# Optimization experiments

Measured on AMD Instinct MI355X. Metric: run time of the kernel, lower is better.

## Reference

```python
import jax, jax.numpy as jnp
import numpy as np

B, G, T, N = 4, 8, 30, 60
CT, CN = 1, 60
FD, IDD = 256, 256
E = FD + IDD          # 512
H = 8                 # (FD+IDD)//head_dim
L = 6                 # num_layers
VP1 = 51              # num_id_vocabulary + 1
PE = 32               # rel_pe_length
DFF = 4 * E


def _ln(x, g, b, eps=1e-5):
    m = x.mean(-1, keepdims=True)
    v = ((x - m) ** 2).mean(-1, keepdims=True)
    return (x - m) / jnp.sqrt(v + eps) * g + b


def _mha(qx, kx, vx, Wqkv, bqkv, Wo, bo, bias, h):
    # torch nn.MultiheadAttention with add_zero_attn=True; bias is additive
    # attn bias of shape [B, h, Lq, Lk+1] (already padded for the zero-attn col).
    e = qx.shape[-1]
    d = e // h
    Wq, Wk, Wv = jnp.split(Wqkv, 3, axis=0)
    bq, bk, bv = jnp.split(bqkv, 3)
    q = qx @ Wq.T + bq
    k = kx @ Wk.T + bk
    v = vx @ Wv.T + bv
    b_, lq, _ = q.shape
    lk = k.shape[1]
    z = jnp.zeros((b_, 1, e), q.dtype)
    k = jnp.concatenate([k, z], axis=1)   # add_zero_attn appends zero key
    v = jnp.concatenate([v, z], axis=1)
    qh = q.reshape(b_, lq, h, d).transpose(0, 2, 1, 3)
    kh = k.reshape(b_, lk + 1, h, d).transpose(0, 2, 1, 3)
    vh = v.reshape(b_, lk + 1, h, d).transpose(0, 2, 1, 3)
    s = jnp.einsum('bhqd,bhkd->bhqk', qh, kh) / jnp.sqrt(jnp.float32(d)) + bias
    p = jax.nn.softmax(s, axis=-1)
    o = jnp.einsum('bhqk,bhkd->bhqd', p, vh).transpose(0, 2, 1, 3).reshape(b_, lq, e)
    return o @ Wo.T + bo


def _forward(tf, uf, ids, tt_, ut_, tm, um, Ww, Wout, rpe,
             saW, sab, saO, saob, sag, sabn,
             caW, cab, caO, caob, cag, cabn,
             f1, fb1, f2, fb2, fg, fbn):
    b, g, t, n, fd = tf.shape
    _, _, ct, cn, _ = uf.shape
    id_dim = Ww.shape[0]
    e = fd + id_dim
    nl = caW.shape[0]
    h = rpe.shape[-1]
    pe = rpe.shape[1]
    # one_hot(label) @ W_word.T == W_word[:, label]
    traj_id = Ww.T[ids]                                        # b g t n id
    unk_id = jnp.broadcast_to(Ww[:, VP1 - 1], (b, g, ct, cn, id_dim))
    traj = jnp.concatenate([tf, traj_id], -1).reshape(b * g, t * n, e)
    unk = jnp.concatenate([uf, unk_id], -1)                    # b g ct cn e

    tt = tt_.reshape(b * g, t * n)
    ut = ut_.reshape(b * g, ct * cn)
    neg = jnp.float32(-jnp.inf)
    zero = jnp.float32(0)
    causal = jnp.where(tt[:, None, :] >= ut[:, :, None], neg, zero)  # bg q k
    kpm = jnp.where(tm.reshape(b * g, t * n), neg, zero)             # bg k
    # torch rel_pos_map[u, t] = u - t; negative torch indices wrap -> mod pe
    rel_idx = (ut[:, :, None] - tt[:, None, :]) % pe                 # bg q k
    sa_bias = jnp.pad(
        jnp.where(um.reshape(b * g * ct, cn), neg, zero)[:, None, None, :],
        ((0, 0), (0, 0), (0, 0), (0, 1)))

    for l in range(nl):
        if l > 0:
            x = unk.reshape(b * g * ct, cn, e)
            y = _mha(x, x, x, saW[l - 1], sab[l - 1], saO[l - 1], saob[l - 1], sa_bias, h)
            unk = _ln(x + y, sag[l - 1], sabn[l - 1]).reshape(b, g, ct, cn, e)
        q = unk.reshape(b * g, ct * cn, e)
        rel = rpe[l][rel_idx]                                  # bg q k h  (gathered rel-PE)
        bias = causal[:, None] + jnp.transpose(rel, (0, 3, 1, 2)) + kpm[:, None, None, :]
        bias = jnp.pad(bias, ((0, 0), (0, 0), (0, 0), (0, 1)))
        y = _mha(q, traj, traj, caW[l], cab[l], caO[l], caob[l], bias, h)
        x = _ln(q + y, cag[l], cabn[l])
        hh = jax.nn.gelu(x @ f1[l].T + fb1[l], approximate=False) @ f2[l].T + fb2[l]
        x = _ln(x + hh, fg[l], fbn[l])
        unk = x.reshape(b, g, ct, cn, e)
    # final layer logits (eval mode): shared embed_to_word head, no bias
    return unk[..., fd:] @ Wout.T


def setup_inputs():
    key = jax.random.key(0)
    ks = iter(jax.random.split(key, 48))
    nrm = lambda shape, s=0.02: jax.random.normal(next(ks), shape, jnp.float32) * s
    return {
        'trajectory_features': jax.random.normal(next(ks), (B, G, T, N, FD), jnp.float32),
        'unknown_features': jax.random.normal(next(ks), (B, G, CT, CN, FD), jnp.float32),
        'trajectory_id_labels': jax.random.randint(next(ks), (B, G, T, N), 0, VP1),
        'trajectory_times': jax.random.randint(next(ks), (B, G, T, N), 0, PE),
        'unknown_times': jax.random.randint(next(ks), (B, G, CT, CN), 0, PE),
        'trajectory_masks': jnp.zeros((B, G, T, N), bool),
        'unknown_masks': jnp.zeros((B, G, CT, CN), bool),
        'use_decoder_checkpoint': 0,
        'W_word': nrm((IDD, VP1), 0.05),
        'W_out': nrm((VP1, IDD), 0.05),
        'rel_pos_embeds': nrm((L, PE, H), 0.1),
        'sa_Wqkv': nrm((L - 1, 3 * E, E)), 'sa_bqkv': jnp.zeros((L - 1, 3 * E)),
        'sa_Wo': nrm((L - 1, E, E)), 'sa_bo': jnp.zeros((L - 1, E)),
        'sa_ln_g': jnp.ones((L - 1, E)), 'sa_ln_b': jnp.zeros((L - 1, E)),
        'ca_Wqkv': nrm((L, 3 * E, E)), 'ca_bqkv': jnp.zeros((L, 3 * E)),
        'ca_Wo': nrm((L, E, E)), 'ca_bo': jnp.zeros((L, E)),
        'ca_ln_g': jnp.ones((L, E)), 'ca_ln_b': jnp.zeros((L, E)),
        'ffn_W1': nrm((L, DFF, E)), 'ffn_b1': jnp.zeros((L, DFF)),
        'ffn_W2': nrm((L, E, DFF)), 'ffn_b2': jnp.zeros((L, E)),
        'ffn_ln_g': jnp.ones((L, E)), 'ffn_ln_b': jnp.zeros((L, E)),
    }


def reference(trajectory_features, unknown_features, trajectory_id_labels,
              trajectory_times, unknown_times, trajectory_masks, unknown_masks,
              use_decoder_checkpoint, W_word, W_out, rel_pos_embeds,
              sa_Wqkv, sa_bqkv, sa_Wo, sa_bo, sa_ln_g, sa_ln_b,
              ca_Wqkv, ca_bqkv, ca_Wo, ca_bo, ca_ln_g, ca_ln_b,
              ffn_W1, ffn_b1, ffn_W2, ffn_b2, ffn_ln_g, ffn_ln_b):
    return _forward(trajectory_features, unknown_features, trajectory_id_labels,
                    trajectory_times, unknown_times, trajectory_masks, unknown_masks,
                    W_word, W_out, rel_pos_embeds,
                    sa_Wqkv, sa_bqkv, sa_Wo, sa_bo, sa_ln_g, sa_ln_b,
                    ca_Wqkv, ca_bqkv, ca_Wo, ca_bo, ca_ln_g, ca_ln_b,
                    ffn_W1, ffn_b1, ffn_W2, ffn_b2, ffn_ln_g, ffn_ln_b)
```

## Files before the change

### kernel.cpp

```cpp
#include <hip/hip_runtime.h>
#include <cmath>

__device__ __forceinline__ float bflo(unsigned int u) {
  union { unsigned int i; float f; } v; v.i = u << 16; return v.f;
}
__device__ __forceinline__ float bfhi(unsigned int u) {
  union { unsigned int i; float f; } v; v.i = u & 0xffff0000u; return v.f;
}
__device__ __forceinline__ float bf2f(unsigned short u) {
  union { unsigned int i; float f; } v; v.i = ((unsigned int)u) << 16; return v.f;
}
__device__ __forceinline__ unsigned short f2bf(float f) {
  union { float f; unsigned int i; } v; v.f = f;
  unsigned int i = v.i;
  return (unsigned short)((i + 0x7fffu + ((i >> 16) & 1u)) >> 16);
}
__device__ __forceinline__ unsigned int pack2bf(float a, float b) {
  return (unsigned int)f2bf(a) | ((unsigned int)f2bf(b) << 16);
}

typedef __attribute__((ext_vector_type(8))) short short8;
typedef __attribute__((ext_vector_type(4))) float floatx4;

__global__ __launch_bounds__(256) void conv_kernel(
    const float* __restrict__ in, unsigned short* __restrict__ out, int n)
{
  int i = (blockIdx.x * 256 + threadIdx.x) << 2;
  if (i >= n) return;
  float4 v = *reinterpret_cast<const float4*>(in + i);
  ushort4 o;
  o.x = f2bf(v.x); o.y = f2bf(v.y); o.z = f2bf(v.z); o.w = f2bf(v.w);
  *reinterpret_cast<ushort4*>(out + i) = o;
}

__global__ __launch_bounds__(256) void build_wwt_kernel(
    const float* __restrict__ Ww, unsigned short* __restrict__ Wwt)
{
  int c = blockIdx.x;
  int r = threadIdx.x;
  Wwt[c * 256 + r] = f2bf(Ww[r * 51 + c]);
}

__global__ __launch_bounds__(512, 4) void gemm256(
    const unsigned short* __restrict__ A,
    const unsigned short* __restrict__ W,
    const float* __restrict__ bias,
    unsigned short* __restrict__ C)
{
  __shared__ __align__(16) unsigned short LA[2][4096];
  __shared__ __align__(16) unsigned short LB[2][8192];
  const int tid = threadIdx.x;
  const int wave = tid >> 6, lane = tid & 63;
  const int quad = lane >> 4, mrow = lane & 15;
  const int wm = wave >> 2, wn = wave & 3;
  const size_t ldK = 512;
  const int nt = 16;

  int f = blockIdx.x;
  {
    const int q = gridDim.x >> 3;
    f = (f & 7) * q + (f >> 3);
  }
  const int bn = (f & 3) << 8;
  const int bm = (f >> 2) << 7;

  floatx4 acc[4][4];
#pragma unroll
  for (int i = 0; i < 4; ++i)
#pragma unroll
    for (int j = 0; j < 4; ++j) acc[i][j] = (floatx4){0.f, 0.f, 0.f, 0.f};

  const int srow = tid >> 2;
  const int sslot = (tid & 3) ^ ((srow >> 1) & 3);

#define STAGE32(p, kelem)                                                            \
  do {                                                                               \
    __builtin_amdgcn_global_load_lds(                                                \
        (const __attribute__((address_space(1))) unsigned int*)(                     \
            A + (size_t)(bm + srow) * ldK + (kelem) + sslot * 8),                    \
        (__attribute__((address_space(3))) unsigned int*)(&LA[(p)][0] + wave * 512), \
        16, 0, 0);                                                                   \
    __builtin_amdgcn_global_load_lds(                                                \
        (const __attribute__((address_space(1))) unsigned int*)(                     \
            W + (size_t)(bn + srow) * ldK + (kelem) + sslot * 8),                    \
        (__attribute__((address_space(3))) unsigned int*)(&LB[(p)][0] + wave * 512), \
        16, 0, 0);                                                                   \
    __builtin_amdgcn_global_load_lds(                                                \
        (const __attribute__((address_space(1))) unsigned int*)(                     \
            W + (size_t)(bn + 128 + srow) * ldK + (kelem) + sslot * 8),              \
        (__attribute__((address_space(3))) unsigned int*)(&LB[(p)][4096] + wave * 512), \
        16, 0, 0);                                                                   \
  } while (0)

  STAGE32(0, 0);
  STAGE32(1, 32);
  asm volatile("s_waitcnt vmcnt(3)" ::: "memory");
  __builtin_amdgcn_s_barrier();

  const int rsw = ((quad ^ ((mrow >> 1) & 3)) << 3);
  const int arowb = wm * 64 + mrow;
  const int brows = wn * 64 + mrow;

  for (int T = 0; T < nt; ++T) {
    const int p = T & 1;
    short8 afr[4], bfr[4];
#pragma unroll
    for (int i = 0; i < 4; ++i)
      afr[i] = *reinterpret_cast<const short8*>(&LA[p][(arowb + i * 16) * 32 + rsw]);
#pragma unroll
    for (int j = 0; j < 4; ++j)
      bfr[j] = *reinterpret_cast<const short8*>(&LB[p][(brows + j * 16) * 32 + rsw]);
    asm volatile("s_waitcnt lgkmcnt(0)" ::: "memory");
    __builtin_amdgcn_s_barrier();
    if (T + 2 < nt) STAGE32(p, (T + 2) * 32);
    __builtin_amdgcn_s_setprio(1);
#pragma unroll
    for (int i = 0; i < 4; ++i)
#pragma unroll
      for (int j = 0; j < 4; ++j)
        acc[i][j] = __builtin_amdgcn_mfma_f32_16x16x32_bf16(afr[i], bfr[j], acc[i][j], 0, 0, 0);
    __builtin_amdgcn_s_setprio(0);
    if (T + 2 < nt) asm volatile("s_waitcnt vmcnt(3)" ::: "memory");
    else            asm volatile("s_waitcnt vmcnt(0)" ::: "memory");
    __builtin_amdgcn_s_barrier();
  }
#undef STAGE32

  const int col0 = lane & 15;
  const int row0 = (lane >> 4) << 2;
#pragma unroll
  for (int i = 0; i < 4; ++i)
#pragma unroll
    for (int j = 0; j < 4; ++j) {
      int col = bn + wn * 64 + j * 16 + col0;
      float bv = bias[col];
#pragma unroll
      for (int r = 0; r < 4; ++r) {
        int row = bm + wm * 64 + i * 16 + row0 + r;
        C[(size_t)row * 1024 + col] = f2bf(acc[i][j][r] + bv);
      }
    }
}

__global__ __launch_bounds__(256) void gemm_mfma(
    const unsigned short* __restrict__ A, int lda,
    const unsigned short* __restrict__ W, int ldw,
    const float* __restrict__ bias,
    void* __restrict__ Cv, int ldc,
    int K, int act, int cbf16, int swz)
{
  __shared__ __align__(16) unsigned short As[2][128 * 32];
  __shared__ __align__(16) unsigned short Bs[2][128 * 32];
  const int tid = threadIdx.x;
  const int wave = tid >> 6, lane = tid & 63;

  int bxi = blockIdx.x, byi = blockIdx.y;
  if (swz) {
    int f = byi * gridDim.x + bxi;
    int q = (gridDim.x * gridDim.y) >> 3;
    f = (f & 7) * q + (f >> 3);
    bxi = f % gridDim.x;
    byi = f / gridDim.x;
  }
  const int bm = byi * 128, bn = bxi * 128;
  const int wm = (wave >> 1) << 6, wn = (wave & 1) << 6;

  floatx4 acc[4][4];
#pragma unroll
  for (int i = 0; i < 4; ++i)
#pragma unroll
    for (int j = 0; j < 4; ++j) acc[i][j] = (floatx4){0.f, 0.f, 0.f, 0.f};

  const int srow = (wave << 5) + (lane >> 2);
  const int chsw = (lane & 3) ^ ((srow >> 1) & 3);
  const int scol = chsw << 3;
  const unsigned short* Ag  = A + (size_t)(bm + srow) * lda + scol;
  const unsigned short* Wg  = W + (size_t)(bn + srow) * ldw + scol;
  const unsigned short* Ag2 = Ag + (size_t)16 * lda;
  const unsigned short* Wg2 = Wg + (size_t)16 * ldw;
  const int ldsw = (wave << 5) * 32;

  const int arow = lane & 15;
  const int rsw  = (arow >> 1) & 3;
  const int chrd = (lane >> 4) ^ rsw;
  const int aoff = (wm + arow) * 32 + (chrd << 3);
  const int boff = (wn + arow) * 32 + (chrd << 3);

  const int nt = K >> 5;

#define STAGE(b, t)                                                                 \
  do {                                                                              \
    const int k0_ = (t) << 5;                                                       \
    __builtin_amdgcn_global_load_lds(                                               \
        (const __attribute__((address_space(1))) unsigned int*)(Ag + k0_),          \
        (__attribute__((address_space(3))) unsigned int*)(As[(b)] + ldsw), 16, 0, 0); \
    __builtin_amdgcn_global_load_lds(                                               \
        (const __attribute__((address_space(1))) unsigned int*)(Ag2 + k0_),         \
        (__attribute__((address_space(3))) unsigned int*)(As[(b)] + ldsw + 16 * 32), 16, 0, 0); \
    __builtin_amdgcn_global_load_lds(                                               \
        (const __attribute__((address_space(1))) unsigned int*)(Wg + k0_),          \
        (__attribute__((address_space(3))) unsigned int*)(Bs[(b)] + ldsw), 16, 0, 0); \
    __builtin_amdgcn_global_load_lds(                                               \
        (const __attribute__((address_space(1))) unsigned int*)(Wg2 + k0_),         \
        (__attribute__((address_space(3))) unsigned int*)(Bs[(b)] + ldsw + 16 * 32), 16, 0, 0); \
  } while (0)

  STAGE(0, 0);
  if (nt > 1) STAGE(1, 1);

  int cur = 0;
  for (int t = 0; t < nt; ++t) {
    if (t + 1 < nt) asm volatile("s_waitcnt vmcnt(4)\n\ts_barrier" ::: "memory");
    else            asm volatile("s_waitcnt vmcnt(0)\n\ts_barrier" ::: "memory");

    short8 af[4], bf[4];
#pragma unroll
    for (int i = 0; i < 4; ++i) {
      af[i] = *reinterpret_cast<const short8*>(&As[cur][aoff + (i << 4) * 32]);
      bf[i] = *reinterpret_cast<const short8*>(&Bs[cur][boff + (i << 4) * 32]);
    }
    asm volatile("s_waitcnt lgkmcnt(0)\n\ts_barrier" ::: "memory");
    if (t + 2 < nt) STAGE(cur, t + 2);

#pragma unroll
    for (int i = 0; i < 4; ++i)
#pragma unroll
      for (int j = 0; j < 4; ++j)
        acc[i][j] = __builtin_amdgcn_mfma_f32_16x16x32_bf16(af[i], bf[j], acc[i][j], 0, 0, 0);
    cur ^= 1;
  }
#undef STAGE

  const int col0 = lane & 15;
  const int row0 = (lane >> 4) << 2;
#pragma unroll
  for (int i = 0; i < 4; ++i) {
#pragma unroll
    for (int j = 0; j < 4; ++j) {
      int col = bn + wn + (j << 4) + col0;
      float bv = bias ? bias[col] : 0.f;
#pragma unroll
      for (int r = 0; r < 4; ++r) {
        int row = bm + wm + (i << 4) + row0 + r;
        float v = acc[i][j][r] + bv;
        if (act) v = 0.5f * v * (1.f + erff(v * 0.70710678f));
        if (cbf16) ((unsigned short*)Cv)[(size_t)row * ldc + col] = f2bf(v);
        else       ((float*)Cv)[(size_t)row * ldc + col] = v;
      }
    }
  }
}

__device__ __forceinline__ float wred_max(float v) {
#pragma unroll
  for (int off = 32; off > 0; off >>= 1) v = fmaxf(v, __shfl_xor(v, off, 64));
  return v;
}
__device__ __forceinline__ float wred_sum(float v) {
#pragma unroll
  for (int off = 32; off > 0; off >>= 1) v += __shfl_xor(v, off, 64);
  return v;
}

#define LDK 72
__global__ __launch_bounds__(512) void attn_mfma_kernel(
    const unsigned short* __restrict__ Qp,
    const unsigned short* __restrict__ KVb,
    unsigned short* __restrict__ O,
    const int* __restrict__ tt, const int* __restrict__ ut,
    const unsigned char* __restrict__ km,
    const float* __restrict__ rel)
{
  const int bg = blockIdx.x >> 3, h = blockIdx.x & 7;
  const int tid = threadIdx.x;
  const int grp = tid >> 8;
  const int wave = (tid >> 6) & 3;
  const int lane = tid & 63;
  const int quad = lane >> 4, mrow = lane & 15;

  __shared__ __align__(16) unsigned short SMEM[6 * 64 * LDK];
  unsigned short* Ks = SMEM + grp * (3 * 64 * LDK);
  unsigned short* Vt = Ks + 64 * LDK;
  unsigned short* Ps = Vt + 64 * LDK;

  const int qa = wave * 16 + mrow;
  const int qc = qa < 60 ? qa : 59;
  const unsigned short* qptr = Qp + (size_t)(bg * 60 + qc) * 512 + h * 64 + quad * 8;
  const short8 af0 = *reinterpret_cast<const short8*>(qptr);
  const short8 af1 = *reinterpret_cast<const short8*>(qptr + 32);

  const float relreg = rel[(lane & 31) * 8 + h];

  int tq[4];
  float m[4], l[4];
  floatx4 acc[4];
#pragma unroll
  for (int r = 0; r < 4; ++r) {
    int qo = wave * 16 + quad * 4 + r;
    tq[r] = ut[bg * 60 + (qo < 60 ? qo : 59)];
    m[r] = grp ? -1e30f : 0.f;
    l[r] = grp ? 0.f : 1.f;
  }
#pragma unroll
  for (int nt = 0; nt < 4; ++nt) acc[nt] = (floatx4){0.f, 0.f, 0.f, 0.f};

  const int sk = tid & 255;
  const int stok = sk >> 2, schk = sk & 3;

  for (int it = 0; it < 15; ++it) {
    const int k0 = (grp + 2 * it) << 6;
    __syncthreads();
    {
      const int key = k0 + stok;
      uint4 kr0 = {0,0,0,0}, kr1 = {0,0,0,0}, vr0 = {0,0,0,0}, vr1 = {0,0,0,0};
      if (key < 1800) {
        const unsigned short* kb = KVb + ((size_t)bg * 1800 + key) * 1024 + h * 64 + schk * 16;
        kr0 = *reinterpret_cast<const uint4*>(kb);
        kr1 = *reinterpret_cast<const uint4*>(kb + 8);
        vr0 = *reinterpret_cast<const uint4*>(kb + 512);
        vr1 = *reinterpret_cast<const uint4*>(kb + 520);
      }
      *reinterpret_cast<uint4*>(&Ks[stok * LDK + schk * 16]) = kr0;
      *reinterpret_cast<uint4*>(&Ks[stok * LDK + schk * 16 + 8]) = kr1;
      unsigned int wv[8] = {vr0.x, vr0.y, vr0.z, vr0.w, vr1.x, vr1.y, vr1.z, vr1.w};
#pragma unroll
      for (int e = 0; e < 16; ++e)
        Vt[(schk * 16 + e) * LDK + stok] = (unsigned short)(wv[e >> 1] >> ((e & 1) * 16));
    }
    int meta = 0x10000;
    {
      int kk = k0 + lane;
      if (kk < 1800) {
        int base = bg * 1800 + kk;
        meta = tt[base] | (km[base] ? 0x10000 : 0);
      }
    }
    __syncthreads();

    floatx4 S[4];
#pragma unroll
    for (int nt = 0; nt < 4; ++nt) {
      const unsigned short* kb = Ks + (nt * 16 + mrow) * LDK + quad * 8;
      short8 b0 = *reinterpret_cast<const short8*>(kb);
      short8 b1 = *reinterpret_cast<const short8*>(kb + 32);
      floatx4 s = (floatx4){0.f, 0.f, 0.f, 0.f};
      s = __builtin_amdgcn_mfma_f32_16x16x32_bf16(af0, b0, s, 0, 0, 0);
      s = __builtin_amdgcn_mfma_f32_16x16x32_bf16(af1, b1, s, 0, 0, 0);
      S[nt] = s;
    }
    int mcol[4];
#pragma unroll
    for (int nt = 0; nt < 4; ++nt)
      mcol[nt] = __builtin_amdgcn_ds_bpermute((nt * 16 + mrow) << 2, meta);
    float sv[4][4];
#pragma unroll
    for (int nt = 0; nt < 4; ++nt) {
      int tk = mcol[nt] & 0xffff;
      int bad0 = mcol[nt] >> 16;
#pragma unroll
      for (int r = 0; r < 4; ++r) {
        float v = S[nt][r] * 0.125f;
        int ridx = (tq[r] - tk) & 31;
        v += __int_as_float(__builtin_amdgcn_ds_bpermute(ridx << 2, __float_as_int(relreg)));
        sv[nt][r] = (bad0 | (tk >= tq[r])) ? -1e30f : v;
      }
    }
#pragma unroll
    for (int r = 0; r < 4; ++r) {
      float rm = fmaxf(fmaxf(sv[0][r], sv[1][r]), fmaxf(sv[2][r], sv[3][r]));
#pragma unroll
      for (int d = 1; d < 16; d <<= 1) rm = fmaxf(rm, __shfl_xor(rm, d, 64));
      float nm = fmaxf(m[r], rm);
      float corr = __expf(m[r] - nm);
      float ps = 0.f;
      const int prow = (wave * 16 + quad * 4 + r) * LDK + mrow;
#pragma unroll
      for (int nt = 0; nt < 4; ++nt) {
        float p = __expf(sv[nt][r] - nm);
        ps += p;
        Ps[prow + nt * 16] = f2bf(p);
      }
#pragma unroll
      for (int d = 1; d < 16; d <<= 1) ps += __shfl_xor(ps, d, 64);
      l[r] = l[r] * corr + ps;
      m[r] = nm;
#pragma unroll
      for (int nt = 0; nt < 4; ++nt) acc[nt][r] *= corr;
    }
    const unsigned short* pp = Ps + (wave * 16 + mrow) * LDK + quad * 8;
    short8 a0 = *reinterpret_cast<const short8*>(pp);
    short8 a1 = *reinterpret_cast<const short8*>(pp + 32);
#pragma unroll
    for (int nt = 0; nt < 4; ++nt) {
      const unsigned short* vb = Vt + (nt * 16 + mrow) * LDK + quad * 8;
      short8 b0 = *reinterpret_cast<const short8*>(vb);
      short8 b1 = *reinterpret_cast<const short8*>(vb + 32);
      acc[nt] = __builtin_amdgcn_mfma_f32_16x16x32_bf16(a0, b0, acc[nt], 0, 0, 0);
      acc[nt] = __builtin_amdgcn_mfma_f32_16x16x32_bf16(a1, b1, acc[nt], 0, 0, 0);
    }
  }

  __syncthreads();
  float* MA = (float*)SMEM;
  float* Ml = (float*)(SMEM + 64 * 68 * 2);
  float* Ll = Ml + 64;
  if (grp == 1) {
#pragma unroll
    for (int r = 0; r < 4; ++r) {
      int row = wave * 16 + quad * 4 + r;
#pragma unroll
      for (int nt = 0; nt < 4; ++nt)
        MA[row * 68 + nt * 16 + mrow] = acc[nt][r];
      if (mrow == 0) { Ml[row] = m[r]; Ll[row] = l[r]; }
    }
  }
  __syncthreads();
  if (grp == 0) {
#pragma unroll
    for (int r = 0; r < 4; ++r) {
      int row = wave * 16 + quad * 4 + r;
      float m1 = Ml[row], l1 = Ll[row];
      float M = fmaxf(m[r], m1);
      float c0 = __expf(m[r] - M), c1 = __expf(m1 - M);
      float invL = 1.f / (l[r] * c0 + l1 * c1);
      if (row < 60) {
        unsigned short* op = O + (size_t)(bg * 60 + row) * 512 + h * 64;
#pragma unroll
        for (int nt = 0; nt < 4; ++nt) {
          float o = (acc[nt][r] * c0 + MA[row * 68 + nt * 16 + mrow] * c1) * invL;
          op[nt * 16 + mrow] = f2bf(o);
        }
      }
    }
  }
}

#define QPB 32
#define QPW 8
__global__ __launch_bounds__(256) void attn2_kernel(
    const unsigned short* __restrict__ Qp, int qs,
    const unsigned short* __restrict__ Kp, int ks,
    const unsigned short* __restrict__ Vp, int vs,
    unsigned short* __restrict__ O, int os, int kLen,
    const unsigned char* __restrict__ kmask)
{
  const int bg = blockIdx.x >> 3;
  const int h  = blockIdx.x & 7;
  const int q0 = blockIdx.y * QPB;
  const int tid = threadIdx.x;
  const int wave = tid >> 6, lane = tid & 63;

  __shared__ float Qs[QPB][68];
  __shared__ float Ks[64][68];
  __shared__ float Vs[64][68];
  __shared__ float Ps[QPB][68];

  {
    int qr = tid >> 3, j = tid & 7;
    int q = q0 + qr;
    float f[8] = {0, 0, 0, 0, 0, 0, 0, 0};
    if (q < 60) {
      uint4 v = *reinterpret_cast<const uint4*>(Qp + (size_t)(bg * 60 + q) * qs + h * 64 + j * 8);
      f[0] = bflo(v.x); f[1] = bfhi(v.x); f[2] = bflo(v.y); f[3] = bfhi(v.y);
      f[4] = bflo(v.z); f[5] = bfhi(v.z); f[6] = bflo(v.w); f[7] = bfhi(v.w);
    }
#pragma unroll
    for (int e = 0; e < 8; ++e) Qs[qr][j * 8 + e] = f[e];
  }

  float m[QPW], l[QPW], acc[QPW];
#pragma unroll
  for (int i = 0; i < QPW; ++i) { m[i] = 0.f; l[i] = 1.f; acc[i] = 0.f; }

  const int std = tid >> 2;
  const int stj = tid & 3;

  for (int k0 = 0; k0 < kLen; k0 += 64) {
    __syncthreads();
    const bool sok = (k0 + std) < kLen;
    {
      const unsigned short* kb = Kp + ((size_t)bg * kLen + k0 + std) * ks + h * 64 + stj * 16;
      float f[16];
#pragma unroll
      for (int e = 0; e < 16; ++e) f[e] = 0.f;
      if (sok) {
        uint4 v0 = *reinterpret_cast<const uint4*>(kb);
        uint4 v1 = *reinterpret_cast<const uint4*>(kb + 8);
        f[0] = bflo(v0.x); f[1] = bfhi(v0.x); f[2]  = bflo(v0.y); f[3]  = bfhi(v0.y);
        f[4] = bflo(v0.z); f[5] = bfhi(v0.z); f[6]  = bflo(v0.w); f[7]  = bfhi(v0.w);
        f[8] = bflo(v1.x); f[9] = bfhi(v1.x); f[10] = bflo(v1.y); f[11] = bfhi(v1.y);
        f[12] = bflo(v1.z); f[13] = bfhi(v1.z); f[14] = bflo(v1.w); f[15] = bfhi(v1.w);
      }
#pragma unroll
      for (int e = 0; e < 16; ++e) Ks[stj * 16 + e][std] = f[e];
    }
    {
      const unsigned short* vb = Vp + ((size_t)bg * kLen + k0 + std) * vs + h * 64;
#pragma unroll
      for (int c = 0; c < 2; ++c) {
        int off = c * 32 + stj * 8;
        float f[8] = {0, 0, 0, 0, 0, 0, 0, 0};
        if (sok) {
          uint4 v = *reinterpret_cast<const uint4*>(vb + off);
          f[0] = bflo(v.x); f[1] = bfhi(v.x); f[2] = bflo(v.y); f[3] = bfhi(v.y);
          f[4] = bflo(v.z); f[5] = bfhi(v.z); f[6] = bflo(v.w); f[7] = bfhi(v.w);
        }
#pragma unroll
        for (int e = 0; e < 8; ++e) Vs[std][off + e] = f[e];
      }
    }
    const int kk = k0 + lane;
    const bool kok = kk < kLen;
    unsigned char kmv = 0;
    if (kok && kmask) kmv = kmask[(size_t)bg * kLen + kk];
    __syncthreads();

    float s[QPW];
#pragma unroll
    for (int i = 0; i < QPW; ++i) s[i] = 0.f;
    for (int d = 0; d < 64; ++d) {
      float kv = Ks[d][lane];
#pragma unroll
      for (int i = 0; i < QPW; ++i)
        s[i] = fmaf(Qs[wave * QPW + i][d], kv, s[i]);
    }

    const int kmax = min(64, kLen - k0);
#pragma unroll
    for (int i = 0; i < QPW; ++i) {
      float svv = s[i] * 0.125f;
      if (kmv || !kok) svv = -1e30f;
      float nm = fmaxf(m[i], wred_max(svv));
      float p = __expf(svv - nm);
      float ts = wred_sum(p);
      float corr = __expf(m[i] - nm);
      l[i] = l[i] * corr + ts;
      acc[i] *= corr;
      m[i] = nm;
      Ps[wave * QPW + i][lane] = p;
    }
    for (int k = 0; k < kmax; ++k) {
      float v = Vs[k][lane];
#pragma unroll
      for (int i = 0; i < QPW; ++i)
        acc[i] = fmaf(Ps[wave * QPW + i][k], v, acc[i]);
    }
  }

#pragma unroll
  for (int i = 0; i < QPW; ++i) {
    int q = q0 + wave * QPW + i;
    if (q < 60)
      O[(size_t)(bg * 60 + q) * os + h * 64 + lane] = f2bf(acc[i] / l[i]);
  }
}

__global__ __launch_bounds__(256) void add_ln_kernel(
    const float* __restrict__ a, const float* __restrict__ b,
    const float* __restrict__ g, const float* __restrict__ be,
    float* __restrict__ o, unsigned short* __restrict__ ob)
{
  const int t = blockIdx.x;
  const int tid = threadIdx.x;
  const int wave = tid >> 6, lane = tid & 63;
  const size_t base = (size_t)t * 512;
  float v0 = a[base + tid] + b[base + tid];
  float v1 = a[base + 256 + tid] + b[base + 256 + tid];
  __shared__ float red[4];
  float s = wred_sum(v0 + v1);
  if (lane == 0) red[wave] = s;
  __syncthreads();
  float mean = (red[0] + red[1] + red[2] + red[3]) * (1.0f / 512.0f);
  float d0 = v0 - mean, d1 = v1 - mean;
  float vs = wred_sum(d0 * d0 + d1 * d1);
  __syncthreads();
  if (lane == 0) red[wave] = vs;
  __syncthreads();
  float var = (red[0] + red[1] + red[2] + red[3]) * (1.0f / 512.0f);
  float rstd = rsqrtf(var + 1e-5f);
  float r0 = d0 * rstd * g[tid] + be[tid];
  float r1 = d1 * rstd * g[256 + tid] + be[256 + tid];
  o[base + tid] = r0;
  o[base + 256 + tid] = r1;
  ob[base + tid] = f2bf(r0);
  ob[base + 256 + tid] = f2bf(r1);
}

__global__ __launch_bounds__(256) void build_traj_kernel(
    const float* __restrict__ tf, const int* __restrict__ ids,
    const unsigned short* __restrict__ Wwt, unsigned short* __restrict__ traj)
{
  int idx = blockIdx.x * 256 + threadIdx.x;
  int tok = idx >> 6;
  int sub = idx & 63;
  uint4 o;
  if (sub < 32) {
    const float* ip = tf + ((size_t)tok << 8) + sub * 8;
    float4 a = *reinterpret_cast<const float4*>(ip);
    float4 b = *reinterpret_cast<const float4*>(ip + 4);
    o.x = pack2bf(a.x, a.y); o.y = pack2bf(a.z, a.w);
    o.z = pack2bf(b.x, b.y); o.w = pack2bf(b.z, b.w);
  } else {
    int id = ids[tok];
    o = *reinterpret_cast<const uint4*>(Wwt + id * 256 + (sub - 32) * 8);
  }
  *reinterpret_cast<uint4*>(traj + ((size_t)tok << 9) + sub * 8) = o;
}

__global__ __launch_bounds__(256) void build_unk_kernel(
    const float* __restrict__ uf, const float* __restrict__ Ww,
    float* __restrict__ x, unsigned short* __restrict__ xb)
{
  int idx = blockIdx.x * 256 + threadIdx.x;
  int tok = idx >> 6;
  int sub = idx & 63;
  float f[8];
  if (sub < 32) {
    const float* ip = uf + ((size_t)tok << 8) + sub * 8;
    float4 a = *reinterpret_cast<const float4*>(ip);
    float4 b = *reinterpret_cast<const float4*>(ip + 4);
    f[0] = a.x; f[1] = a.y; f[2] = a.z; f[3] = a.w;
    f[4] = b.x; f[5] = b.y; f[6] = b.z; f[7] = b.w;
  } else {
    const float* wp = Ww + (size_t)((sub - 32) * 8) * 51 + 50;
#pragma unroll
    for (int e = 0; e < 8; ++e) f[e] = wp[e * 51];
  }
  size_t base = ((size_t)tok << 9) + sub * 8;
  float4 x0 = {f[0], f[1], f[2], f[3]};
  float4 x1 = {f[4], f[5], f[6], f[7]};
  *reinterpret_cast<float4*>(x + base) = x0;
  *reinterpret_cast<float4*>(x + base + 4) = x1;
  uint4 o;
  o.x = pack2bf(f[0], f[1]); o.y = pack2bf(f[2], f[3]);
  o.z = pack2bf(f[4], f[5]); o.w = pack2bf(f[6], f[7]);
  *reinterpret_cast<uint4*>(xb + base) = o;
}

__global__ __launch_bounds__(64) void head_kernel(
    const float* __restrict__ x, const float* __restrict__ Wout, float* __restrict__ out)
{
  const int t = blockIdx.x;
  const int tid = threadIdx.x;
  __shared__ float xs[256];
  for (int i = tid; i < 256; i += 64) xs[i] = x[(size_t)t * 512 + 256 + i];
  __syncthreads();
  if (tid < 51) {
    const float* w = Wout + tid * 256;
    float s = 0.f;
    for (int k = 0; k < 256; ++k) s = fmaf(xs[k], w[k], s);
    out[t * 51 + tid] = s;
  }
}

extern "C" void kernel_launch(void* const* d_in, const int* in_sizes, int n_in,
                              void* d_out, int out_size, void* d_ws, size_t ws_size,
                              hipStream_t stream) {
  const float* tf  = (const float*)d_in[0];
  const float* uf  = (const float*)d_in[1];
  const int*   ids = (const int*)d_in[2];
  const int*   tt  = (const int*)d_in[3];
  const int*   ut  = (const int*)d_in[4];
  const unsigned char* tm = (const unsigned char*)d_in[5];
  const unsigned char* um = (const unsigned char*)d_in[6];
  const float* Ww   = (const float*)d_in[8];
  const float* Wout = (const float*)d_in[9];
  const float* rpe  = (const float*)d_in[10];
  const float* saW  = (const float*)d_in[11];
  const float* sab  = (const float*)d_in[12];
  const float* saO  = (const float*)d_in[13];
  const float* saob = (const float*)d_in[14];
  const float* sag  = (const float*)d_in[15];
  const float* sabn = (const float*)d_in[16];
  const float* caW  = (const float*)d_in[17];
  const float* cab  = (const float*)d_in[18];
  const float* caO  = (const float*)d_in[19];
  const float* caob = (const float*)d_in[20];
  const float* cag  = (const float*)d_in[21];
  const float* cabn = (const float*)d_in[22];
  const float* f1   = (const float*)d_in[23];
  const float* fb1  = (const float*)d_in[24];
  const float* f2   = (const float*)d_in[25];
  const float* fb2  = (const float*)d_in[26];
  const float* fg   = (const float*)d_in[27];
  const float* fbn  = (const float*)d_in[28];

  unsigned short* trajb = (unsigned short*)d_ws;
  unsigned short* KVb   = trajb + (size_t)29491200;
  unsigned short* qkvb  = KVb   + (size_t)58982400;
  unsigned short* hb    = qkvb  + (size_t)2949120;
  unsigned short* xb    = hb    + (size_t)3932160;
  float* x    = (float*)(xb + (size_t)983040);
  float* ybuf = x + (size_t)983040;
  unsigned short* wtail = (unsigned short*)(ybuf + (size_t)983040);

  const size_t NEED = (size_t)200540160 + (size_t)24117248 * 2 + 32768;
  const bool pre = ws_size >= NEED;
  unsigned short* wsa  = wtail;
  unsigned short* wsaO = wsa  + (size_t)3932160;
  unsigned short* wca  = wsaO + (size_t)1310720;
  unsigned short* wcaO = wca  + (size_t)4718592;
  unsigned short* wf1  = wcaO + (size_t)1572864;
  unsigned short* wf2  = wf1  + (size_t)6291456;
  unsigned short* Wwt  = wf2  + (size_t)6291456;
  unsigned short* wconv = wtail;
  unsigned short* WwtF  = wconv + (size_t)1048576;

  if (pre) {
    conv_kernel<<<dim3(3840), dim3(256), 0, stream>>>(saW, wsa, 3932160);
    conv_kernel<<<dim3(1280), dim3(256), 0, stream>>>(saO, wsaO, 1310720);
    conv_kernel<<<dim3(4608), dim3(256), 0, stream>>>(caW, wca, 4718592);
    conv_kernel<<<dim3(1536), dim3(256), 0, stream>>>(caO, wcaO, 1572864);
    conv_kernel<<<dim3(6144), dim3(256), 0, stream>>>(f1, wf1, 6291456);
    conv_kernel<<<dim3(6144), dim3(256), 0, stream>>>(f2, wf2, 6291456);
  }
  unsigned short* wwt = pre ? Wwt : WwtF;
  build_wwt_kernel<<<dim3(51), dim3(256), 0, stream>>>(Ww, wwt);

  build_traj_kernel<<<dim3(14400), dim3(256), 0, stream>>>(tf, ids, wwt, trajb);
  build_unk_kernel<<<dim3(480), dim3(256), 0, stream>>>(uf, Ww, x, xb);

  for (int l = 0; l < 6; ++l) {
    if (l > 0) {
      int sl = l - 1;
      const unsigned short* wq;
      if (pre) wq = wsa + (size_t)sl * 786432;
      else {
        conv_kernel<<<dim3(768), dim3(256), 0, stream>>>(saW + (size_t)sl * 786432, wconv, 786432);
        wq = wconv;
      }
      gemm_mfma<<<dim3(12, 15), dim3(256), 0, stream>>>(
          xb, 512, wq, 512, sab + sl * 1536, qkvb, 1536, 512, 0, 1, 0);
      attn2_kernel<<<dim3(256, 2), dim3(256), 0, stream>>>(
          qkvb, 1536, qkvb + 512, 1536, qkvb + 1024, 1536, hb, 512, 60, um);
      const unsigned short* wo;
      if (pre) wo = wsaO + (size_t)sl * 262144;
      else {
        conv_kernel<<<dim3(256), dim3(256), 0, stream>>>(saO + (size_t)sl * 262144, wconv, 262144);
        wo = wconv;
      }
      gemm_mfma<<<dim3(4, 15), dim3(256), 0, stream>>>(
          hb, 512, wo, 512, saob + sl * 512, ybuf, 512, 512, 0, 0, 0);
      add_ln_kernel<<<dim3(1920), dim3(256), 0, stream>>>(x, ybuf, sag + sl * 512, sabn + sl * 512, x, xb);
    }
    const unsigned short* wqkv;
    if (pre) wqkv = wca + (size_t)l * 786432;
    else {
      conv_kernel<<<dim3(768), dim3(256), 0, stream>>>(caW + (size_t)l * 786432, wconv, 786432);
      wqkv = wconv;
    }
    gemm256<<<dim3(1800), dim3(512), 0, stream>>>(
        trajb, wqkv + 262144, cab + l * 1536 + 512, KVb);
    gemm_mfma<<<dim3(4, 15), dim3(256), 0, stream>>>(
        xb, 512, wqkv, 512, cab + l * 1536, qkvb, 512, 512, 0, 1, 0);
    attn_mfma_kernel<<<dim3(256), dim3(512), 0, stream>>>(
        qkvb, KVb, hb, tt, ut, tm, rpe + l * 256);
    const unsigned short* wco;
    if (pre) wco = wcaO + (size_t)l * 262144;
    else {
      conv_kernel<<<dim3(256), dim3(256), 0, stream>>>(caO + (size_t)l * 262144, wconv, 262144);
      wco = wconv;
    }
    gemm_mfma<<<dim3(4, 15), dim3(256), 0, stream>>>(
        hb, 512, wco, 512, caob + l * 512, ybuf, 512, 512, 0, 0, 0);
    add_ln_kernel<<<dim3(1920), dim3(256), 0, stream>>>(x, ybuf, cag + l * 512, cabn + l * 512, x, xb);
    const unsigned short* w1;
    if (pre) w1 = wf1 + (size_t)l * 1048576;
    else {
      conv_kernel<<<dim3(1024), dim3(256), 0, stream>>>(f1 + (size_t)l * 1048576, wconv, 1048576);
      w1 = wconv;
    }
    gemm_mfma<<<dim3(16, 15), dim3(256), 0, stream>>>(
        xb, 512, w1, 512, fb1 + l * 2048, hb, 2048, 512, 1, 1, 0);
    const unsigned short* w2;
    if (pre) w2 = wf2 + (size_t)l * 1048576;
    else {
      conv_kernel<<<dim3(1024), dim3(256), 0, stream>>>(f2 + (size_t)l * 1048576, wconv, 1048576);
      w2 = wconv;
    }
    gemm_mfma<<<dim3(4, 15), dim3(256), 0, stream>>>(
        hb, 2048, w2, 2048, fb2 + l * 512, ybuf, 512, 2048, 0, 0, 0);
    add_ln_kernel<<<dim3(1920), dim3(256), 0, stream>>>(x, ybuf, fg + l * 512, fbn + l * 512, x, xb);
  }
  head_kernel<<<dim3(1920), dim3(64), 0, stream>>>(x, Wout, (float*)d_out);
}
```

Measured before the change: 1.822 ms.

## Batch all layers' cross-attention K/V projections into one GEMM launch

The cross-attention K/V projection of the trajectory tokens does not depend on the layer's activations. So all six layers' K/V GEMMs are issued as one large gemm256 launch before the layer loop, each writing its own per-layer KV buffer. The aim is fewer launches and smaller tail inefficiency per layer. The cost is a much larger workspace, and the path is only enabled when the workspace is big enough. The launch bound is also relaxed to 2 blocks per CU, which lets the compiler use more registers.

Result: slower. 1.951 ms (+7.1%).

```diff
diff --git a/kernel.cpp b/kernel.cpp
--- a/kernel.cpp
+++ b/kernel.cpp
@@ -41,11 +41,12 @@
   Wwt[c * 256 + r] = f2bf(Ww[r * 51 + c]);
 }
 
-__global__ __launch_bounds__(512, 4) void gemm256(
+__global__ __launch_bounds__(512, 2) void gemm256(
     const unsigned short* __restrict__ A,
-    const unsigned short* __restrict__ W,
-    const float* __restrict__ bias,
-    unsigned short* __restrict__ C)
+    const unsigned short* __restrict__ W,  size_t wstr,
+    const float* __restrict__ bias,        int bstr,
+    unsigned short* __restrict__ C,        size_t cstr,
+    int nx)
 {
   __shared__ __align__(16) unsigned short LA[2][4096];
   __shared__ __align__(16) unsigned short LB[2][8192];
@@ -61,8 +62,14 @@
     const int q = gridDim.x >> 3;
     f = (f & 7) * q + (f >> 3);
   }
-  const int bn = (f & 3) << 8;
-  const int bm = (f >> 2) << 7;
+  const int bn_t = f % nx;
+  const int bm = (f / nx) << 7;
+  const int bn = bn_t << 8;
+  const int l  = bn >> 10;
+  const int bncol = bn & 1023;
+  const unsigned short* Wl = W + (size_t)l * wstr;
+  const float* biasl = bias + (size_t)l * bstr;
+  unsigned short* Cl = C + (size_t)l * cstr;
 
   floatx4 acc[4][4];
 #pragma unroll
@@ -82,12 +89,12 @@
         16, 0, 0);                                                                   \
     __builtin_amdgcn_global_load_lds(                                                \
         (const __attribute__((address_space(1))) unsigned int*)(                     \
-            W + (size_t)(bn + srow) * ldK + (kelem) + sslot * 8),                    \
+            Wl + (size_t)(bncol + srow) * ldK + (kelem) + sslot * 8),                \
         (__attribute__((address_space(3))) unsigned int*)(&LB[(p)][0] + wave * 512), \
         16, 0, 0);                                                                   \
     __builtin_amdgcn_global_load_lds(                                                \
         (const __attribute__((address_space(1))) unsigned int*)(                     \
-            W + (size_t)(bn + 128 + srow) * ldK + (kelem) + sslot * 8),              \
+            Wl + (size_t)(bncol + 128 + srow) * ldK + (kelem) + sslot * 8),          \
         (__attribute__((address_space(3))) unsigned int*)(&LB[(p)][4096] + wave * 512), \
         16, 0, 0);                                                                   \
   } while (0)
@@ -132,12 +139,12 @@
   for (int i = 0; i < 4; ++i)
 #pragma unroll
     for (int j = 0; j < 4; ++j) {
-      int col = bn + wn * 64 + j * 16 + col0;
-      float bv = bias[col];
+      int col = bncol + wn * 64 + j * 16 + col0;
+      float bv = biasl[col];
 #pragma unroll
       for (int r = 0; r < 4; ++r) {
         int row = bm + wm * 64 + i * 16 + row0 + r;
-        C[(size_t)row * 1024 + col] = f2bf(acc[i][j][r] + bv);
+        Cl[(size_t)row * 1024 + col] = f2bf(acc[i][j][r] + bv);
       }
     }
 }
@@ -685,17 +692,22 @@
   const float* fg   = (const float*)d_in[27];
   const float* fbn  = (const float*)d_in[28];
 
+  const size_t KV1 = (size_t)58982400;
   unsigned short* trajb = (unsigned short*)d_ws;
-  unsigned short* KVb   = trajb + (size_t)29491200;
-  unsigned short* qkvb  = KVb   + (size_t)58982400;
-  unsigned short* hb    = qkvb  + (size_t)2949120;
-  unsigned short* xb    = hb    + (size_t)3932160;
+  const size_t NEED_BATCH = (size_t)850000000;
+  const bool batched = ws_size >= NEED_BATCH;
+  const int NKV = batched ? 6 : 1;
+
+  unsigned short* KVb  = trajb + (size_t)29491200;
+  unsigned short* qkvb = KVb   + KV1 * NKV;
+  unsigned short* hb   = qkvb  + (size_t)2949120;
+  unsigned short* xb   = hb    + (size_t)3932160;
   float* x    = (float*)(xb + (size_t)983040);
   float* ybuf = x + (size_t)983040;
   unsigned short* wtail = (unsigned short*)(ybuf + (size_t)983040);
 
   const size_t NEED = (size_t)200540160 + (size_t)24117248 * 2 + 32768;
-  const bool pre = ws_size >= NEED;
+  const bool pre = batched || ws_size >= NEED;
   unsigned short* wsa  = wtail;
   unsigned short* wsaO = wsa  + (size_t)3932160;
   unsigned short* wca  = wsaO + (size_t)1310720;
@@ -720,6 +732,11 @@
   build_traj_kernel<<<dim3(14400), dim3(256), 0, stream>>>(tf, ids, wwt, trajb);
   build_unk_kernel<<<dim3(480), dim3(256), 0, stream>>>(uf, Ww, x, xb);
 
+  if (batched) {
+    gemm256<<<dim3(10800), dim3(512), 0, stream>>>(
+        trajb, wca + 262144, (size_t)786432, cab + 512, 1536, KVb, KV1, 24);
+  }
+
   for (int l = 0; l < 6; ++l) {
     if (l > 0) {
       int sl = l - 1;
@@ -749,12 +766,15 @@
       conv_kernel<<<dim3(768), dim3(256), 0, stream>>>(caW + (size_t)l * 786432, wconv, 786432);
       wqkv = wconv;
     }
-    gemm256<<<dim3(1800), dim3(512), 0, stream>>>(
-        trajb, wqkv + 262144, cab + l * 1536 + 512, KVb);
+    unsigned short* KVl = KVb + KV1 * (batched ? l : 0);
+    if (!batched) {
+      gemm256<<<dim3(1800), dim3(512), 0, stream>>>(
+          trajb, wqkv + 262144, (size_t)0, cab + l * 1536 + 512, 0, KVl, (size_t)0, 4);
+    }
     gemm_mfma<<<dim3(4, 15), dim3(256), 0, stream>>>(
         xb, 512, wqkv, 512, cab + l * 1536, qkvb, 512, 512, 0, 1, 0);
     attn_mfma_kernel<<<dim3(256), dim3(512), 0, stream>>>(
-        qkvb, KVb, hb, tt, ut, tm, rpe + l * 256);
+        qkvb, KVl, hb, tt, ut, tm, rpe + l * 256);
     const unsigned short* wco;
     if (pre) wco = wcaO + (size_t)l * 262144;
     else {
```
